# Optimization experiments

Measured on AMD Instinct MI355X. Metric: run time of the kernel, lower is better.

## Reference

```python
import jax, jax.numpy as jnp
import numpy as np

MIN_NORM = 1e-15
N = 10000        # num_nodes
E = 320000       # num edges (avg degree 32)
F_IN = 512       # in_features
HID = 256        # hardcoded encoder hidden dim
D_HYP = 2        # Poincare embedding dim
HEIGHT = 2
MAX_SIZE = 0.999
MIN_SCALE = HEIGHT * (MAX_SIZE / (HEIGHT + 1))  # = 0.666, scale clamp lower bound
MAX_SCALE = MAX_SIZE


def setup_inputs() -> dict:
    key = jax.random.key(0)
    ks = jax.random.split(key, 5)
    feature = jax.random.normal(ks[0], (N, F_IN), jnp.float32)
    edge_index = jax.random.randint(ks[1], (2, E), 0, N, dtype=jnp.int64)
    W1 = jax.random.normal(ks[2], (F_IN, HID), jnp.float32) / np.sqrt(F_IN).astype(np.float32)
    b1 = jnp.zeros((HID,), jnp.float32)
    W2 = jax.random.normal(ks[3], (HID, D_HYP), jnp.float32) / np.sqrt(HID).astype(np.float32)
    b2 = jnp.zeros((D_HYP,), jnp.float32)
    scale = jnp.ones((1,), jnp.float32)  # init_size overridden to 1.0 in __init__
    return {"feature": feature, "edge_index": edge_index, "W1": W1, "b1": b1,
            "W2": W2, "b2": b2, "scale": scale}


def _gcn_agg(h, src, dst):
    # symmetric-normalized edge_index gather/aggregate (message passing)
    deg = jax.ops.segment_sum(jnp.ones((src.shape[0],), h.dtype), dst, num_segments=N)
    deg = jnp.maximum(deg, 1.0)
    norm = jax.lax.rsqrt(deg[src] * deg[dst])            # [E]
    msg = h[src] * norm[:, None]                          # [E, C] gather (irregular)
    return jax.ops.segment_sum(msg, dst, num_segments=N)  # [N, C] scatter-add


def reference(feature, edge_index, W1, b1, W2, b2, scale):
    src, dst = edge_index[0], edge_index[1]
    # 2-layer graph encoder (linear -> aggregate -> relu, linear -> aggregate)
    h = jax.nn.relu(_gcn_agg(feature @ W1 + b1, src, dst))   # [N, HID]
    u = _gcn_agg(h @ W2 + b2, src, dst)                      # [N, D_HYP] tangent at origin
    # lift to Lorentz model (k=-1) via expmap0: x = [cosh|u|, sinh|u| * u/|u|]
    un = jnp.maximum(jnp.linalg.norm(u, axis=-1, keepdims=True), MIN_NORM)
    x_l = jnp.concatenate([jnp.cosh(un), jnp.sinh(un) * u / un], axis=-1)  # [N, D_HYP+1]
    # Lorentz -> Poincare: p = x_space / (1 + x_time)
    p = x_l[:, 1:] / (1.0 + x_l[:, :1])
    # normalize: F.normalize(p, dim=-1) * scale.clamp(min_size, max_size)
    pn = jnp.maximum(jnp.linalg.norm(p, axis=-1, keepdims=True), 1e-12)
    s = jnp.clip(scale, MIN_SCALE, MAX_SCALE)
    p = p / pn * s
    # project onto Poincare ball of curvature k=-1 with eps=MIN_NORM
    norm = jnp.maximum(jnp.linalg.norm(p, axis=-1, keepdims=True), MIN_NORM)
    maxnorm = 1.0 - MIN_NORM
    return jnp.where(norm > maxnorm, p / norm * maxnorm, p)
```

## Files before the change

kernel.cpp:

```cpp
#include <hip/hip_runtime.h>
#include <math.h>

#define N_NODES 10000
#define N_EDGES 320000
#define F_IN 512
#define HID 256
#define PAD_DEG 80
#define LDSTR 40
#define N_GTILES 158
#define BUILD_BLKS ((N_EDGES + 255) / 256)

typedef _Float16 half8 __attribute__((ext_vector_type(8)));
typedef float floatx4 __attribute__((ext_vector_type(4)));

__device__ __forceinline__ void fma4(float4& acc, float s, const float4& v) {
    acc.x += s * v.x; acc.y += s * v.y; acc.z += s * v.z; acc.w += s * v.w;
}


__global__ __launch_bounds__(256) void k_pre(const float* __restrict__ W1,
                                             int* __restrict__ count,
                                             _Float16* __restrict__ Bt_hi,
                                             _Float16* __restrict__ Bt_lo) {
    int i = blockIdx.x * blockDim.x + threadIdx.x;
    if (i < 10240) count[i] = 0;
    int k = i >> 8, n = i & 255;
    float v = W1[i];
    _Float16 hi = (_Float16)v;
    Bt_hi[n * F_IN + k] = hi;
    Bt_lo[n * F_IN + k] = (_Float16)(v - (float)hi);
}


__global__ __launch_bounds__(256) void k_combo(const float* __restrict__ A,
                                               const _Float16* __restrict__ Bt_hi,
                                               const _Float16* __restrict__ Bt_lo,
                                               const float* __restrict__ b1,
                                               float* __restrict__ h0,
                                               const int* __restrict__ ei,
                                               int* __restrict__ count,
                                               int* __restrict__ csr) {
    __shared__ _Float16 As_hi[128 * LDSTR], As_lo[128 * LDSTR];
    __shared__ _Float16 Bs_hi[128 * LDSTR], Bs_lo[128 * LDSTR];
    const int tid = threadIdx.x;

    if (blockIdx.x >= N_GTILES) {
        int e = (blockIdx.x - N_GTILES) * 256 + tid;
        if (e < N_EDGES) {
            int src = ei[e];
            int dst = ei[N_EDGES + e];
            int pos = atomicAdd(&count[dst], 1);
            csr[dst * PAD_DEG + pos] = src;
        }
        return;
    }

    const int lane = tid & 63, w = tid >> 6;
    const int wm = (w >> 1) * 64, wn = (w & 1) * 64;
    const int quad = lane >> 4, l15 = lane & 15;
    const int r = tid >> 1, c = (tid & 1) << 4;
    const int t = blockIdx.x;
    const int row0 = (t >> 1) * 128, col0 = (t & 1) * 128;
    floatx4 acc[4][4] = {};

    const int arow = row0 + r;
    const float* Aptr = A + (size_t)arow * F_IN + c;
    const _Float16* Bh = Bt_hi + (size_t)(col0 + r) * F_IN + c;
    const _Float16* Bl = Bt_lo + (size_t)(col0 + r) * F_IN + c;

    for (int k0 = 0; k0 < F_IN; k0 += 32) {
        float av[16];
        if (arow < N_NODES) {
            #pragma unroll
            for (int q = 0; q < 4; ++q) {
                float4 v = *(const float4*)(Aptr + k0 + q * 4);
                av[q * 4 + 0] = v.x; av[q * 4 + 1] = v.y;
                av[q * 4 + 2] = v.z; av[q * 4 + 3] = v.w;
            }
        } else {
            #pragma unroll
            for (int i = 0; i < 16; ++i) av[i] = 0.f;
        }
        half8 hhi[2], hlo[2];
        #pragma unroll
        for (int i = 0; i < 16; ++i) {
            _Float16 h = (_Float16)av[i];
            hhi[i >> 3][i & 7] = h;
            hlo[i >> 3][i & 7] = (_Float16)(av[i] - (float)h);
        }
        *(half8*)&As_hi[r * LDSTR + c]     = hhi[0];
        *(half8*)&As_hi[r * LDSTR + c + 8] = hhi[1];
        *(half8*)&As_lo[r * LDSTR + c]     = hlo[0];
        *(half8*)&As_lo[r * LDSTR + c + 8] = hlo[1];
        *(half8*)&Bs_hi[r * LDSTR + c]     = *(const half8*)(Bh + k0);
        *(half8*)&Bs_hi[r * LDSTR + c + 8] = *(const half8*)(Bh + k0 + 8);
        *(half8*)&Bs_lo[r * LDSTR + c]     = *(const half8*)(Bl + k0);
        *(half8*)&Bs_lo[r * LDSTR + c + 8] = *(const half8*)(Bl + k0 + 8);
        __syncthreads();
        half8 a_hi[4], a_lo[4];
        #pragma unroll
        for (int mi = 0; mi < 4; ++mi) {
            int mr = wm + mi * 16 + l15;
            a_hi[mi] = *(half8*)&As_hi[mr * LDSTR + quad * 8];
            a_lo[mi] = *(half8*)&As_lo[mr * LDSTR + quad * 8];
        }
        #pragma unroll
        for (int ni = 0; ni < 4; ++ni) {
            int nr = wn + ni * 16 + l15;
            half8 b_hi = *(half8*)&Bs_hi[nr * LDSTR + quad * 8];
            half8 b_lo = *(half8*)&Bs_lo[nr * LDSTR + quad * 8];
            #pragma unroll
            for (int mi = 0; mi < 4; ++mi) {
                acc[mi][ni] = __builtin_amdgcn_mfma_f32_16x16x32_f16(a_hi[mi], b_hi, acc[mi][ni], 0, 0, 0);
                acc[mi][ni] = __builtin_amdgcn_mfma_f32_16x16x32_f16(a_hi[mi], b_lo, acc[mi][ni], 0, 0, 0);
                acc[mi][ni] = __builtin_amdgcn_mfma_f32_16x16x32_f16(a_lo[mi], b_hi, acc[mi][ni], 0, 0, 0);
            }
        }
        __syncthreads();
    }
    #pragma unroll
    for (int mi = 0; mi < 4; ++mi)
        #pragma unroll
        for (int ni = 0; ni < 4; ++ni) {
            int colb = col0 + wn + ni * 16 + l15;
            float bias = b1[colb];
            #pragma unroll
            for (int reg = 0; reg < 4; ++reg) {
                int rowb = row0 + wm + mi * 16 + quad * 4 + reg;
                if (rowb < N_NODES) h0[(size_t)rowb * HID + colb] = acc[mi][ni][reg] + bias;
            }
        }
}


__global__ __launch_bounds__(256) void k_agg1(const float* __restrict__ h0,
                                              const int* __restrict__ csr,
                                              const int* __restrict__ count,
                                              const float* __restrict__ W2,
                                              const float* __restrict__ b2,
                                              float* __restrict__ u0) {
    __shared__ int2 nb[4][PAD_DEG];
    const int wid = threadIdx.x >> 6;
    const int lane = threadIdx.x & 63;
    const int n = blockIdx.x * 4 + wid;
    const int deg = count[n];
    const float degd = (float)(deg > 0 ? deg : 1);
    const int* row = csr + (size_t)n * PAD_DEG;
    for (int j = lane; j < deg; j += 64) {
        int s = row[j];
        int cs = count[s];
        float wq = rsqrtf((float)(cs > 0 ? cs : 1) * degd);
        nb[wid][j] = make_int2(s, __float_as_int(wq));
    }
    __syncthreads();

    const int off = lane << 2;
    float4 acc0 = {0,0,0,0}, acc1 = {0,0,0,0}, acc2 = {0,0,0,0}, acc3 = {0,0,0,0};
    int j = 0;
    for (; j + 8 <= deg; j += 8) {
        int2 e0 = nb[wid][j+0], e1 = nb[wid][j+1], e2 = nb[wid][j+2], e3 = nb[wid][j+3];
        int2 e4 = nb[wid][j+4], e5 = nb[wid][j+5], e6 = nb[wid][j+6], e7 = nb[wid][j+7];
        float4 v0 = *(const float4*)(h0 + ((size_t)e0.x << 8) + off);
        float4 v1 = *(const float4*)(h0 + ((size_t)e1.x << 8) + off);
        float4 v2 = *(const float4*)(h0 + ((size_t)e2.x << 8) + off);
        float4 v3 = *(const float4*)(h0 + ((size_t)e3.x << 8) + off);
        float4 v4 = *(const float4*)(h0 + ((size_t)e4.x << 8) + off);
        float4 v5 = *(const float4*)(h0 + ((size_t)e5.x << 8) + off);
        float4 v6 = *(const float4*)(h0 + ((size_t)e6.x << 8) + off);
        float4 v7 = *(const float4*)(h0 + ((size_t)e7.x << 8) + off);
        fma4(acc0, __int_as_float(e0.y), v0);
        fma4(acc1, __int_as_float(e1.y), v1);
        fma4(acc2, __int_as_float(e2.y), v2);
        fma4(acc3, __int_as_float(e3.y), v3);
        fma4(acc0, __int_as_float(e4.y), v4);
        fma4(acc1, __int_as_float(e5.y), v5);
        fma4(acc2, __int_as_float(e6.y), v6);
        fma4(acc3, __int_as_float(e7.y), v7);
    }
    for (; j < deg; ++j) {
        int2 e = nb[wid][j];
        float4 v = *(const float4*)(h0 + ((size_t)e.x << 8) + off);
        fma4(acc0, __int_as_float(e.y), v);
    }
    acc0.x += acc1.x + acc2.x + acc3.x;
    acc0.y += acc1.y + acc2.y + acc3.y;
    acc0.z += acc1.z + acc2.z + acc3.z;
    acc0.w += acc1.w + acc2.w + acc3.w;
    acc0.x = fmaxf(acc0.x, 0.f); acc0.y = fmaxf(acc0.y, 0.f);
    acc0.z = fmaxf(acc0.z, 0.f); acc0.w = fmaxf(acc0.w, 0.f);
    float4 wa = *(const float4*)(W2 + (lane << 3));
    float4 wb = *(const float4*)(W2 + (lane << 3) + 4);
    float p0 = acc0.x * wa.x + acc0.y * wa.z + acc0.z * wb.x + acc0.w * wb.z;
    float p1 = acc0.x * wa.y + acc0.y * wa.w + acc0.z * wb.y + acc0.w * wb.w;
    #pragma unroll
    for (int o = 32; o > 0; o >>= 1) {
        p0 += __shfl_down(p0, o);
        p1 += __shfl_down(p1, o);
    }
    if (lane == 0) {
        u0[2 * n]     = p0 + b2[0];
        u0[2 * n + 1] = p1 + b2[1];
    }
}


__global__ __launch_bounds__(256) void k_agg2(const float* __restrict__ u0,
                                              const int* __restrict__ csr,
                                              const int* __restrict__ count,
                                              const float* __restrict__ scale,
                                              float* __restrict__ out) {
    int n = blockIdx.x * 4 + (threadIdx.x >> 6);
    int lane = threadIdx.x & 63;
    if (n >= N_NODES) return;
    int deg = count[n];
    float degd = (float)(deg > 0 ? deg : 1);
    const int* row = csr + (size_t)n * PAD_DEG;
    float a0 = 0.f, a1 = 0.f;
    for (int j = lane; j < deg; j += 64) {
        int s = row[j];
        int cs = count[s];
        float wq = rsqrtf((float)(cs > 0 ? cs : 1) * degd);
        float2 uv = *(const float2*)(u0 + 2 * (size_t)s);
        a0 += wq * uv.x;
        a1 += wq * uv.y;
    }
    #pragma unroll
    for (int o = 32; o > 0; o >>= 1) {
        a0 += __shfl_down(a0, o);
        a1 += __shfl_down(a1, o);
    }
    if (lane == 0) {
        float un = fmaxf(sqrtf(a0 * a0 + a1 * a1), 1e-15f);
        float t = tanhf(0.5f * un) / un;
        float p0 = a0 * t, p1 = a1 * t;
        float pn = fmaxf(sqrtf(p0 * p0 + p1 * p1), 1e-12f);
        float s = fminf(fmaxf(scale[0], 0.666f), 0.999f);
        p0 = p0 / pn * s; p1 = p1 / pn * s;
        float nn = fmaxf(sqrtf(p0 * p0 + p1 * p1), 1e-15f);
        if (nn > 1.0f) { p0 = p0 / nn; p1 = p1 / nn; }
        out[2 * n]     = p0;
        out[2 * n + 1] = p1;
    }
}


extern "C" void kernel_launch(void* const* d_in, const int* in_sizes, int n_in,
                              void* d_out, int out_size, void* d_ws, size_t ws_size,
                              hipStream_t stream) {
    const float* feature = (const float*)d_in[0];
    const int*   ei      = (const int*)d_in[1];
    const float* W1      = (const float*)d_in[2];
    const float* b1      = (const float*)d_in[3];
    const float* W2      = (const float*)d_in[4];
    const float* b2      = (const float*)d_in[5];
    const float* scale   = (const float*)d_in[6];
    float* out = (float*)d_out;

    char* W = (char*)d_ws;
    int*      count = (int*)W;
    int*      csr   = (int*)(W + 40960);
    float*    h0    = (float*)(W + 3240960);
    float*    u0    = (float*)(W + 13480960);
    _Float16* Bt_hi = (_Float16*)(W + 13560960);
    _Float16* Bt_lo = (_Float16*)(W + 13823104);

    k_pre<<<dim3(512), dim3(256), 0, stream>>>(W1, count, Bt_hi, Bt_lo);
    k_combo<<<dim3(N_GTILES + BUILD_BLKS), dim3(256), 0, stream>>>(
        feature, Bt_hi, Bt_lo, b1, h0, ei, count, csr);
    k_agg1<<<dim3((N_NODES + 3) / 4), dim3(256), 0, stream>>>(h0, csr, count, W2, b2, u0);
    k_agg2<<<dim3((N_NODES + 3) / 4), dim3(256), 0, stream>>>(u0, csr, count, scale, out);
}
```

Baseline: 160.1 us.

## Double-buffer LDS tiles and prefetch next K-slice in GEMM

Result: faster. 150.3 us (-6.1%).

```diff
diff --git a/kernel.cpp b/kernel.cpp
--- a/kernel.cpp
+++ b/kernel.cpp
@@ -40,8 +40,8 @@
                                                const int* __restrict__ ei,
                                                int* __restrict__ count,
                                                int* __restrict__ csr) {
-    __shared__ _Float16 As_hi[128 * LDSTR], As_lo[128 * LDSTR];
-    __shared__ _Float16 Bs_hi[128 * LDSTR], Bs_lo[128 * LDSTR];
+    __shared__ _Float16 As_hi[2][128 * LDSTR], As_lo[2][128 * LDSTR];
+    __shared__ _Float16 Bs_hi[2][128 * LDSTR], Bs_lo[2][128 * LDSTR];
     const int tid = threadIdx.x;
 
     if (blockIdx.x >= N_GTILES) {
@@ -64,22 +64,28 @@
     floatx4 acc[4][4] = {};
 
     const int arow = row0 + r;
+    const bool aval = arow < N_NODES;
     const float* Aptr = A + (size_t)arow * F_IN + c;
     const _Float16* Bh = Bt_hi + (size_t)(col0 + r) * F_IN + c;
     const _Float16* Bl = Bt_lo + (size_t)(col0 + r) * F_IN + c;
 
+    float4 apf[4] = {{0,0,0,0},{0,0,0,0},{0,0,0,0},{0,0,0,0}};
+    half8 bhpf[2], blpf[2];
+
+    if (aval) {
+        #pragma unroll
+        for (int q = 0; q < 4; ++q) apf[q] = *(const float4*)(Aptr + q * 4);
+    }
+    bhpf[0] = *(const half8*)(Bh);     bhpf[1] = *(const half8*)(Bh + 8);
+    blpf[0] = *(const half8*)(Bl);     blpf[1] = *(const half8*)(Bl + 8);
+
+    int buf = 0;
     for (int k0 = 0; k0 < F_IN; k0 += 32) {
         float av[16];
-        if (arow < N_NODES) {
-            #pragma unroll
-            for (int q = 0; q < 4; ++q) {
-                float4 v = *(const float4*)(Aptr + k0 + q * 4);
-                av[q * 4 + 0] = v.x; av[q * 4 + 1] = v.y;
-                av[q * 4 + 2] = v.z; av[q * 4 + 3] = v.w;
-            }
-        } else {
-            #pragma unroll
-            for (int i = 0; i < 16; ++i) av[i] = 0.f;
+        #pragma unroll
+        for (int q = 0; q < 4; ++q) {
+            av[4 * q + 0] = apf[q].x; av[4 * q + 1] = apf[q].y;
+            av[4 * q + 2] = apf[q].z; av[4 * q + 3] = apf[q].w;
         }
         half8 hhi[2], hlo[2];
         #pragma unroll
@@ -88,27 +94,41 @@
             hhi[i >> 3][i & 7] = h;
             hlo[i >> 3][i & 7] = (_Float16)(av[i] - (float)h);
         }
-        *(half8*)&As_hi[r * LDSTR + c]     = hhi[0];
-        *(half8*)&As_hi[r * LDSTR + c + 8] = hhi[1];
-        *(half8*)&As_lo[r * LDSTR + c]     = hlo[0];
-        *(half8*)&As_lo[r * LDSTR + c + 8] = hlo[1];
-        *(half8*)&Bs_hi[r * LDSTR + c]     = *(const half8*)(Bh + k0);
-        *(half8*)&Bs_hi[r * LDSTR + c + 8] = *(const half8*)(Bh + k0 + 8);
-        *(half8*)&Bs_lo[r * LDSTR + c]     = *(const half8*)(Bl + k0);
-        *(half8*)&Bs_lo[r * LDSTR + c + 8] = *(const half8*)(Bl + k0 + 8);
+        *(half8*)&As_hi[buf][r * LDSTR + c]     = hhi[0];
+        *(half8*)&As_hi[buf][r * LDSTR + c + 8] = hhi[1];
+        *(half8*)&As_lo[buf][r * LDSTR + c]     = hlo[0];
+        *(half8*)&As_lo[buf][r * LDSTR + c + 8] = hlo[1];
+        *(half8*)&Bs_hi[buf][r * LDSTR + c]     = bhpf[0];
+        *(half8*)&Bs_hi[buf][r * LDSTR + c + 8] = bhpf[1];
+        *(half8*)&Bs_lo[buf][r * LDSTR + c]     = blpf[0];
+        *(half8*)&Bs_lo[buf][r * LDSTR + c + 8] = blpf[1];
+
+        if (k0 + 32 < F_IN) {
+            if (aval) {
+                #pragma unroll
+                for (int q = 0; q < 4; ++q)
+                    apf[q] = *(const float4*)(Aptr + k0 + 32 + q * 4);
+            }
+            bhpf[0] = *(const half8*)(Bh + k0 + 32);
+            bhpf[1] = *(const half8*)(Bh + k0 + 40);
+            blpf[0] = *(const half8*)(Bl + k0 + 32);
+            blpf[1] = *(const half8*)(Bl + k0 + 40);
+        }
+
         __syncthreads();
+
         half8 a_hi[4], a_lo[4];
         #pragma unroll
         for (int mi = 0; mi < 4; ++mi) {
             int mr = wm + mi * 16 + l15;
-            a_hi[mi] = *(half8*)&As_hi[mr * LDSTR + quad * 8];
-            a_lo[mi] = *(half8*)&As_lo[mr * LDSTR + quad * 8];
+            a_hi[mi] = *(half8*)&As_hi[buf][mr * LDSTR + quad * 8];
+            a_lo[mi] = *(half8*)&As_lo[buf][mr * LDSTR + quad * 8];
         }
         #pragma unroll
         for (int ni = 0; ni < 4; ++ni) {
             int nr = wn + ni * 16 + l15;
-            half8 b_hi = *(half8*)&Bs_hi[nr * LDSTR + quad * 8];
-            half8 b_lo = *(half8*)&Bs_lo[nr * LDSTR + quad * 8];
+            half8 b_hi = *(half8*)&Bs_hi[buf][nr * LDSTR + quad * 8];
+            half8 b_lo = *(half8*)&Bs_lo[buf][nr * LDSTR + quad * 8];
             #pragma unroll
             for (int mi = 0; mi < 4; ++mi) {
                 acc[mi][ni] = __builtin_amdgcn_mfma_f32_16x16x32_f16(a_hi[mi], b_hi, acc[mi][ni], 0, 0, 0);
@@ -116,7 +136,7 @@
                 acc[mi][ni] = __builtin_amdgcn_mfma_f32_16x16x32_f16(a_lo[mi], b_hi, acc[mi][ni], 0, 0, 0);
             }
         }
-        __syncthreads();
+        buf ^= 1;
     }
     #pragma unroll
     for (int mi = 0; mi < 4; ++mi)
```

## Replace LDS-tiled GEMM with register-direct MFMA loads and deepen gather unroll

Applied to the files above, without the earlier changes.

New measurement: 161.1 us. Within noise of the previous version (+0.6%).

```diff
diff --git a/kernel.cpp b/kernel.cpp
--- a/kernel.cpp
+++ b/kernel.cpp
@@ -6,8 +6,7 @@
 #define F_IN 512
 #define HID 256
 #define PAD_DEG 80
-#define LDSTR 40
-#define N_GTILES 158
+#define N_GEMM_BLKS 157
 #define BUILD_BLKS ((N_EDGES + 255) / 256)
 
 typedef _Float16 half8 __attribute__((ext_vector_type(8)));
@@ -32,20 +31,18 @@
 }
 
 
-__global__ __launch_bounds__(256) void k_combo(const float* __restrict__ A,
-                                               const _Float16* __restrict__ Bt_hi,
-                                               const _Float16* __restrict__ Bt_lo,
-                                               const float* __restrict__ b1,
-                                               float* __restrict__ h0,
-                                               const int* __restrict__ ei,
-                                               int* __restrict__ count,
-                                               int* __restrict__ csr) {
-    __shared__ _Float16 As_hi[128 * LDSTR], As_lo[128 * LDSTR];
-    __shared__ _Float16 Bs_hi[128 * LDSTR], Bs_lo[128 * LDSTR];
+__global__ __launch_bounds__(256) void k_main(const float* __restrict__ A,
+                                              const _Float16* __restrict__ Bt_hi,
+                                              const _Float16* __restrict__ Bt_lo,
+                                              const float* __restrict__ b1,
+                                              float* __restrict__ h0,
+                                              const int* __restrict__ ei,
+                                              int* __restrict__ count,
+                                              int* __restrict__ csr) {
     const int tid = threadIdx.x;
 
-    if (blockIdx.x >= N_GTILES) {
-        int e = (blockIdx.x - N_GTILES) * 256 + tid;
+    if (blockIdx.x >= N_GEMM_BLKS) {
+        int e = (blockIdx.x - N_GEMM_BLKS) * 256 + tid;
         if (e < N_EDGES) {
             int src = ei[e];
             int dst = ei[N_EDGES + e];
@@ -56,77 +53,89 @@
     }
 
     const int lane = tid & 63, w = tid >> 6;
-    const int wm = (w >> 1) * 64, wn = (w & 1) * 64;
     const int quad = lane >> 4, l15 = lane & 15;
-    const int r = tid >> 1, c = (tid & 1) << 4;
-    const int t = blockIdx.x;
-    const int row0 = (t >> 1) * 128, col0 = (t & 1) * 128;
+    const int row0 = blockIdx.x * 64;
+    const int colw = w * 64;
     floatx4 acc[4][4] = {};
 
-    const int arow = row0 + r;
-    const float* Aptr = A + (size_t)arow * F_IN + c;
-    const _Float16* Bh = Bt_hi + (size_t)(col0 + r) * F_IN + c;
-    const _Float16* Bl = Bt_lo + (size_t)(col0 + r) * F_IN + c;
-
-    for (int k0 = 0; k0 < F_IN; k0 += 32) {
-        float av[16];
-        if (arow < N_NODES) {
-            #pragma unroll
-            for (int q = 0; q < 4; ++q) {
-                float4 v = *(const float4*)(Aptr + k0 + q * 4);
-                av[q * 4 + 0] = v.x; av[q * 4 + 1] = v.y;
-                av[q * 4 + 2] = v.z; av[q * 4 + 3] = v.w;
-            }
-        } else {
-            #pragma unroll
-            for (int i = 0; i < 16; ++i) av[i] = 0.f;
-        }
-        half8 hhi[2], hlo[2];
-        #pragma unroll
-        for (int i = 0; i < 16; ++i) {
-            _Float16 h = (_Float16)av[i];
-            hhi[i >> 3][i & 7] = h;
-            hlo[i >> 3][i & 7] = (_Float16)(av[i] - (float)h);
-        }
-        *(half8*)&As_hi[r * LDSTR + c]     = hhi[0];
-        *(half8*)&As_hi[r * LDSTR + c + 8] = hhi[1];
-        *(half8*)&As_lo[r * LDSTR + c]     = hlo[0];
-        *(half8*)&As_lo[r * LDSTR + c + 8] = hlo[1];
-        *(half8*)&Bs_hi[r * LDSTR + c]     = *(const half8*)(Bh + k0);
-        *(half8*)&Bs_hi[r * LDSTR + c + 8] = *(const half8*)(Bh + k0 + 8);
-        *(half8*)&Bs_lo[r * LDSTR + c]     = *(const half8*)(Bl + k0);
-        *(half8*)&Bs_lo[r * LDSTR + c + 8] = *(const half8*)(Bl + k0 + 8);
-        __syncthreads();
-        half8 a_hi[4], a_lo[4];
+    const float*    aptr[4];
+    const _Float16* bhptr[4];
+    const _Float16* blptr[4];
+    #pragma unroll
+    for (int mi = 0; mi < 4; ++mi) {
+        int ar = row0 + mi * 16 + l15;
+        if (ar >= N_NODES) ar = N_NODES - 1;
+        aptr[mi] = A + (size_t)ar * F_IN + quad * 8;
+    }
+    #pragma unroll
+    for (int ni = 0; ni < 4; ++ni) {
+        int col = colw + ni * 16 + l15;
+        bhptr[ni] = Bt_hi + (size_t)col * F_IN + quad * 8;
+        blptr[ni] = Bt_lo + (size_t)col * F_IN + quad * 8;
+    }
+
+    float4 apf[4][2];
+    half8  bhp[4], blp[4];
+    #pragma unroll
+    for (int mi = 0; mi < 4; ++mi) {
+        apf[mi][0] = *(const float4*)(aptr[mi]);
+        apf[mi][1] = *(const float4*)(aptr[mi] + 4);
+    }
+    #pragma unroll
+    for (int ni = 0; ni < 4; ++ni) {
+        bhp[ni] = *(const half8*)(bhptr[ni]);
+        blp[ni] = *(const half8*)(blptr[ni]);
+    }
+
+    #pragma unroll
+    for (int kk = 0; kk < 16; ++kk) {
+        half8 ah[4], al[4];
         #pragma unroll
         for (int mi = 0; mi < 4; ++mi) {
-            int mr = wm + mi * 16 + l15;
-            a_hi[mi] = *(half8*)&As_hi[mr * LDSTR + quad * 8];
-            a_lo[mi] = *(half8*)&As_lo[mr * LDSTR + quad * 8];
-        }
+            float av[8] = {apf[mi][0].x, apf[mi][0].y, apf[mi][0].z, apf[mi][0].w,
+                           apf[mi][1].x, apf[mi][1].y, apf[mi][1].z, apf[mi][1].w};
+            #pragma unroll
+            for (int j = 0; j < 8; ++j) {
+                _Float16 h = (_Float16)av[j];
+                ah[mi][j] = h;
+                al[mi][j] = (_Float16)(av[j] - (float)h);
+            }
+        }
+        if (kk < 15) {
+            const int k1 = (kk + 1) * 32;
+            #pragma unroll
+            for (int mi = 0; mi < 4; ++mi) {
+                apf[mi][0] = *(const float4*)(aptr[mi] + k1);
+                apf[mi][1] = *(const float4*)(aptr[mi] + k1 + 4);
+            }
+        }
+        #pragma unroll
+        for (int ni = 0; ni < 4; ++ni)
+            #pragma unroll
+            for (int mi = 0; mi < 4; ++mi) {
+                acc[mi][ni] = __builtin_amdgcn_mfma_f32_16x16x32_f16(ah[mi], bhp[ni], acc[mi][ni], 0, 0, 0);
+                acc[mi][ni] = __builtin_amdgcn_mfma_f32_16x16x32_f16(ah[mi], blp[ni], acc[mi][ni], 0, 0, 0);
+                acc[mi][ni] = __builtin_amdgcn_mfma_f32_16x16x32_f16(al[mi], bhp[ni], acc[mi][ni], 0, 0, 0);
+            }
+        if (kk < 15) {
+            const int k1 = (kk + 1) * 32;
+            #pragma unroll
+            for (int ni = 0; ni < 4; ++ni) {
+                bhp[ni] = *(const half8*)(bhptr[ni] + k1);
+                blp[ni] = *(const half8*)(blptr[ni] + k1);
+            }
+        }
+    }
+
+    #pragma unroll
+    for (int mi = 0; mi < 4; ++mi)
         #pragma unroll
         for (int ni = 0; ni < 4; ++ni) {
-            int nr = wn + ni * 16 + l15;
-            half8 b_hi = *(half8*)&Bs_hi[nr * LDSTR + quad * 8];
-            half8 b_lo = *(half8*)&Bs_lo[nr * LDSTR + quad * 8];
-            #pragma unroll
-            for (int mi = 0; mi < 4; ++mi) {
-                acc[mi][ni] = __builtin_amdgcn_mfma_f32_16x16x32_f16(a_hi[mi], b_hi, acc[mi][ni], 0, 0, 0);
-                acc[mi][ni] = __builtin_amdgcn_mfma_f32_16x16x32_f16(a_hi[mi], b_lo, acc[mi][ni], 0, 0, 0);
-                acc[mi][ni] = __builtin_amdgcn_mfma_f32_16x16x32_f16(a_lo[mi], b_hi, acc[mi][ni], 0, 0, 0);
-            }
-        }
-        __syncthreads();
-    }
-    #pragma unroll
-    for (int mi = 0; mi < 4; ++mi)
-        #pragma unroll
-        for (int ni = 0; ni < 4; ++ni) {
-            int colb = col0 + wn + ni * 16 + l15;
+            int colb = colw + ni * 16 + l15;
             float bias = b1[colb];
             #pragma unroll
             for (int reg = 0; reg < 4; ++reg) {
-                int rowb = row0 + wm + mi * 16 + quad * 4 + reg;
+                int rowb = row0 + mi * 16 + quad * 4 + reg;
                 if (rowb < N_NODES) h0[(size_t)rowb * HID + colb] = acc[mi][ni][reg] + bias;
             }
         }
@@ -157,25 +166,32 @@
     const int off = lane << 2;
     float4 acc0 = {0,0,0,0}, acc1 = {0,0,0,0}, acc2 = {0,0,0,0}, acc3 = {0,0,0,0};
     int j = 0;
-    for (; j + 8 <= deg; j += 8) {
+    for (; j + 16 <= deg; j += 16) {
+        int2 e[16];
+        #pragma unroll
+        for (int q = 0; q < 16; ++q) e[q] = nb[wid][j + q];
+        float4 v[16];
+        #pragma unroll
+        for (int q = 0; q < 16; ++q)
+            v[q] = *(const float4*)(h0 + ((size_t)e[q].x << 8) + off);
+        #pragma unroll
+        for (int q = 0; q < 16; q += 4) {
+            fma4(acc0, __int_as_float(e[q + 0].y), v[q + 0]);
+            fma4(acc1, __int_as_float(e[q + 1].y), v[q + 1]);
+            fma4(acc2, __int_as_float(e[q + 2].y), v[q + 2]);
+            fma4(acc3, __int_as_float(e[q + 3].y), v[q + 3]);
+        }
+    }
+    for (; j + 4 <= deg; j += 4) {
         int2 e0 = nb[wid][j+0], e1 = nb[wid][j+1], e2 = nb[wid][j+2], e3 = nb[wid][j+3];
-        int2 e4 = nb[wid][j+4], e5 = nb[wid][j+5], e6 = nb[wid][j+6], e7 = nb[wid][j+7];
         float4 v0 = *(const float4*)(h0 + ((size_t)e0.x << 8) + off);
         float4 v1 = *(const float4*)(h0 + ((size_t)e1.x << 8) + off);
         float4 v2 = *(const float4*)(h0 + ((size_t)e2.x << 8) + off);
         float4 v3 = *(const float4*)(h0 + ((size_t)e3.x << 8) + off);
-        float4 v4 = *(const float4*)(h0 + ((size_t)e4.x << 8) + off);
-        float4 v5 = *(const float4*)(h0 + ((size_t)e5.x << 8) + off);
-        float4 v6 = *(const float4*)(h0 + ((size_t)e6.x << 8) + off);
-        float4 v7 = *(const float4*)(h0 + ((size_t)e7.x << 8) + off);
         fma4(acc0, __int_as_float(e0.y), v0);
         fma4(acc1, __int_as_float(e1.y), v1);
         fma4(acc2, __int_as_float(e2.y), v2);
         fma4(acc3, __int_as_float(e3.y), v3);
-        fma4(acc0, __int_as_float(e4.y), v4);
-        fma4(acc1, __int_as_float(e5.y), v5);
-        fma4(acc2, __int_as_float(e6.y), v6);
-        fma4(acc3, __int_as_float(e7.y), v7);
     }
     for (; j < deg; ++j) {
         int2 e = nb[wid][j];
@@ -265,7 +281,7 @@
     _Float16* Bt_lo = (_Float16*)(W + 13823104);
 
     k_pre<<<dim3(512), dim3(256), 0, stream>>>(W1, count, Bt_hi, Bt_lo);
-    k_combo<<<dim3(N_GTILES + BUILD_BLKS), dim3(256), 0, stream>>>(
+    k_main<<<dim3(N_GEMM_BLKS + BUILD_BLKS), dim3(256), 0, stream>>>(
         feature, Bt_hi, Bt_lo, b1, h0, ei, count, csr);
     k_agg1<<<dim3((N_NODES + 3) / 4), dim3(256), 0, stream>>>(h0, csr, count, W2, b2, u0);
     k_agg2<<<dim3((N_NODES + 3) / 4), dim3(256), 0, stream>>>(u0, csr, count, scale, out);
```
